# Performance work log

Hardware: AMD Instinct MI355X
Metric: run time of the kernel (lower is better)

Reference implementation:

```python
import jax, jax.numpy as jnp
import numpy as np

N_CIR, N_DIS, D, H = 585, 88, 128, 8
E_CC, E_DD = 20000, 3000
EPS = 1e-16


def _gcn(x, src, dst, ew, W, b, N):
    # PyG GCNConv: add self-loops (weight 1), symmetric normalization, x @ W, scatter-add, + bias
    loop = jnp.arange(N)
    s = jnp.concatenate([src, loop])
    d = jnp.concatenate([dst, loop])
    w = jnp.concatenate([ew, jnp.ones((N,), ew.dtype)])
    deg = jax.ops.segment_sum(w, d, num_segments=N)
    dinv = jnp.where(deg > 0, jax.lax.rsqrt(deg), 0.0)
    norm = dinv[s] * w * dinv[d]                      # [E+N]
    h = x @ W                                         # [N,D]
    out = jax.ops.segment_sum(h[s] * norm[:, None], d, num_segments=N)
    return out + b


def _gat(x, src, dst, ea, W, a_src, a_dst, a_edge, We, b, N):
    # PyG GATConv(heads=H, concat=False, edge_dim=1): self-loops with mean edge_attr fill,
    # leaky_relu attention logits, segment softmax over destination, mean over heads, + bias
    loop = jnp.arange(N)
    s = jnp.concatenate([src, loop])
    d = jnp.concatenate([dst, loop])
    ea = jnp.concatenate([ea, jnp.broadcast_to(ea.mean(0, keepdims=True), (N, ea.shape[1]))], 0)
    h = (x @ W).reshape(N, H, D)                      # [N,H,D]
    e = (ea @ We).reshape(-1, H, D)                   # [E+N,H,D]
    alpha = (h * a_src).sum(-1)[s] + (h * a_dst).sum(-1)[d] + (e * a_edge).sum(-1)
    alpha = jax.nn.leaky_relu(alpha, 0.2)             # [E+N,H]
    amax = jax.ops.segment_max(alpha, d, num_segments=N)
    ex = jnp.exp(alpha - amax[d])
    den = jax.ops.segment_sum(ex, d, num_segments=N)
    alpha = ex / (den[d] + EPS)
    out = jax.ops.segment_sum(h[s] * alpha[:, :, None], d, num_segments=N)  # [N,H,D]
    return out.mean(1) + b


def _branch(x, edges, mat, gw1, gb1, aw, asrc, adst, aedge, awe, ab, gw2, gb2, N):
    src, dst = edges[0], edges[1]
    ew = mat[src, dst]                                # gather edge weights from dense matrix
    f1 = jax.nn.relu(_gcn(x, src, dst, ew, gw1, gb1, N))
    att = jax.nn.relu(_gat(f1, src, dst, ew[:, None], aw, asrc, adst, aedge, awe, ab, N))
    f2 = jax.nn.relu(_gcn(att, src, dst, ew, gw2, gb2, N))
    return f1, f2


def _cnn(f1, f2, Wk, b):
    # Conv2d(2,256,(128,1)) over [1,2,128,N] == per-node GEMM over (2,128) then view/transpose
    Xv = jnp.stack([f1.T, f2.T])                      # [2,D,N]
    return jnp.einsum('ock,ckn->no', Wk[..., 0], Xv) + b  # [N,256]


def setup_inputs():
    ks = jax.random.split(jax.random.key(0), 24)
    rn = lambda i, sh, s=1.0: jax.random.normal(ks[i], sh, jnp.float32) * s
    w = 0.08  # ~glorot scale for fan-in 128
    return {
        'x_cir': rn(0, (N_CIR, D)),
        'x_dis': rn(1, (N_DIS, D)),
        'cc_matrix': jax.random.uniform(ks[2], (N_CIR, N_CIR), jnp.float32),
        'dd_matrix': jax.random.uniform(ks[3], (N_DIS, N_DIS), jnp.float32),
        'gcn_c1_w': rn(4, (D, D), w), 'gcn_c1_b': jnp.zeros((D,), jnp.float32),
        'gat_c_w': rn(5, (D, H * D), w), 'gat_c_asrc': rn(6, (H, D), w),
        'gat_c_adst': rn(7, (H, D), w), 'gat_c_aedge': rn(8, (H, D), w),
        'gat_c_we': rn(9, (1, H * D), w), 'gat_c_b': jnp.zeros((D,), jnp.float32),
        'gcn_c2_w': rn(10, (D, D), w), 'gcn_c2_b': jnp.zeros((D,), jnp.float32),
        'gcn_d1_w': rn(11, (D, D), w), 'gcn_d1_b': jnp.zeros((D,), jnp.float32),
        'gat_d_w': rn(12, (D, H * D), w), 'gat_d_asrc': rn(13, (H, D), w),
        'gat_d_adst': rn(14, (H, D), w), 'gat_d_aedge': rn(15, (H, D), w),
        'gat_d_we': rn(16, (1, H * D), w), 'gat_d_b': jnp.zeros((D,), jnp.float32),
        'gcn_d2_w': rn(17, (D, D), w), 'gcn_d2_b': jnp.zeros((D,), jnp.float32),
        'conv_c_w': rn(18, (256, 2, D, 1), w), 'conv_c_b': jnp.zeros((256,), jnp.float32),
        'conv_d_w': rn(19, (256, 2, D, 1), w), 'conv_d_b': jnp.zeros((256,), jnp.float32),
        'cc_edges': jax.random.randint(ks[20], (2, E_CC), 0, N_CIR),
        'dd_edges': jax.random.randint(ks[21], (2, E_DD), 0, N_DIS),
    }


def reference(x_cir, x_dis, cc_matrix, dd_matrix,
              gcn_c1_w, gcn_c1_b, gat_c_w, gat_c_asrc, gat_c_adst, gat_c_aedge, gat_c_we, gat_c_b,
              gcn_c2_w, gcn_c2_b,
              gcn_d1_w, gcn_d1_b, gat_d_w, gat_d_asrc, gat_d_adst, gat_d_aedge, gat_d_we, gat_d_b,
              gcn_d2_w, gcn_d2_b,
              conv_c_w, conv_c_b, conv_d_w, conv_d_b,
              cc_edges, dd_edges):
    c1, c2 = _branch(x_cir, cc_edges, cc_matrix, gcn_c1_w, gcn_c1_b, gat_c_w, gat_c_asrc,
                     gat_c_adst, gat_c_aedge, gat_c_we, gat_c_b, gcn_c2_w, gcn_c2_b, N_CIR)
    d1, d2 = _branch(x_dis, dd_edges, dd_matrix, gcn_d1_w, gcn_d1_b, gat_d_w, gat_d_asrc,
                     gat_d_adst, gat_d_aedge, gat_d_we, gat_d_b, gcn_d2_w, gcn_d2_b, N_DIS)
    cir_fea = _cnn(c1, c2, conv_c_w, conv_c_b)        # [585,256]
    dis_fea = _cnn(d1, d2, conv_d_w, conv_d_b)        # [88,256]
    return cir_fea @ dis_fea.T, cir_fea, dis_fea
```

## Files before the change

kernel.cpp:

```cpp
#include <hip/hip_runtime.h>

constexpr int NCIR = 585;
constexpr int NDIS = 88;
constexpr int NT   = NCIR + NDIS;
constexpr int DIM  = 128;
constexpr int NH   = 8;
constexpr int ECC  = 20000;
constexpr int EDD  = 3000;
constexpr int ET   = ECC + EDD;
constexpr int CO   = 256;
constexpr int CAP  = 256;
constexpr int F1C  = (NCIR + 3) / 4;
constexpr int F1D  = (NDIS + 3) / 4;
constexpr int NG   = F1C + F1D;
constexpr int GBK  = (ET + 255) / 256;
constexpr int GEMB = (NT + 1) / 2;

__device__ __forceinline__ int decode_cnt(unsigned raw){
  return (int)(raw >= 0xA0000000u ? raw - 0xAAAAAAAAu : raw);
}

struct P {
  const float *x_c, *x_d, *mat_c, *mat_d;
  const float *g1w_c, *g1b_c, *aw_c, *as_c, *ad_c, *ae_c, *we_c, *ab_c, *g2w_c, *g2b_c;
  const float *g1w_d, *g1b_d, *aw_d, *as_d, *ad_d, *ae_d, *we_d, *ab_d, *g2w_d, *g2b_d;
  const float *cw_c, *cb_c, *cw_d, *cb_d;
  const int *csrc, *cdst, *dsrc, *ddst;
  float *hs, *hd, *h, *f1, *hg, *fill_w, *psc, *psd, *wdeg;
  unsigned *cnt;
  int *fill_s;
  float *out_score, *out_cir, *out_dis;
};

__global__ __launch_bounds__(256) void k_gg(P p){
  __shared__ float r0[256], r1[256];
  int b = blockIdx.x, t = threadIdx.x;
  if (b < GBK){
    int e = b * 256 + t;
    float wc = 0.0f, wdv = 0.0f;
    if (e < ET){
      float w; int s, d;
      if (e < ECC){
        s = p.csrc[e]; d = p.cdst[e];
        w = p.mat_c[s * NCIR + d]; wc = w;
      } else {
        int el = e - ECC;
        s = NCIR + p.dsrc[el]; d = NCIR + p.ddst[el];
        w = p.mat_d[(s - NCIR) * NDIS + (d - NCIR)]; wdv = w;
      }
      int pos = decode_cnt(atomicAdd(&p.cnt[d], 1u));
      if (pos < CAP){
        p.fill_s[d * CAP + pos] = s;
        p.fill_w[d * CAP + pos] = w;
      }
      atomicAdd(&p.wdeg[d], w);
    }
    r0[t] = wc; r1[t] = wdv;
    __syncthreads();
    for (int st = 128; st; st >>= 1){
      if (t < st){ r0[t] += r0[t + st]; r1[t] += r1[t + st]; }
      __syncthreads();
    }
    if (t == 0){ p.psc[b] = r0[0]; p.psd[b] = r1[0]; }
  } else {
    int ub = (b - GBK) * 2;
    int n = t >> 7, k = t & 127;
    int u = ub + n;
    bool ok = u < NT;
    if (ok){
      int br = u >= NCIR;
      r0[n * DIM + k] = br ? p.x_d[(u - NCIR) * DIM + k] : p.x_c[u * DIM + k];
    }
    __syncthreads();
    if (ok){
      const float* W = (u >= NCIR) ? p.g1w_d : p.g1w_c;
      float acc = 0.0f;
      #pragma unroll 8
      for (int c = 0; c < DIM; ++c) acc += r0[n * DIM + c] * W[c * DIM + k];
      p.h[u * DIM + k] = acc;
    }
  }
}

__global__ __launch_bounds__(256) void k_aggproj(P p){
  __shared__ int   deg4[4];
  __shared__ float dv4[4];
  __shared__ int   s4[4][CAP];
  __shared__ float nrm4[4][CAP];
  __shared__ float a_sh[4][DIM];
  __shared__ float wred[4][8];
  int b = blockIdx.x, t = threadIdx.x;
  int ng = b >> 2, ct = b & 3;
  int base, count, br;
  if (ng < F1C){ base = ng * 4; count = min(4, NCIR - base); br = 0; }
  else { base = NCIR + (ng - F1C) * 4; count = 4; br = 1; }
  if (t < 4){
    if (t < count){
      int u = base + t;
      deg4[t] = min(decode_cnt(p.cnt[u]), CAP);
      dv4[t]  = rsqrtf(1.0f + p.wdeg[u]);
    } else deg4[t] = 0;
  }
  __syncthreads();
  for (int idx = t; idx < 4 * CAP; idx += 256){
    int nn = idx >> 8, j = idx & (CAP - 1);
    if (j < deg4[nn]){
      int u = base + nn;
      int s = p.fill_s[u * CAP + j];
      s4[nn][j] = s;
      nrm4[nn][j] = rsqrtf(1.0f + p.wdeg[s]) * p.fill_w[u * CAP + j] * dv4[nn];
    }
  }
  __syncthreads();
  const float* B1 = br ? p.g1b_d : p.g1b_c;
  int n2 = t >> 7, k = t & 127;
  for (int r = 0; r < 2; ++r){
    int nn = n2 + r * 2;
    float v = 0.0f;
    if (nn < count){
      int u = base + nn;
      float dvu = dv4[nn];
      float acc = B1[k] + p.h[u * DIM + k] * dvu * dvu;
      int deg = deg4[nn];
      #pragma unroll 4
      for (int j = 0; j < deg; ++j)
        acc += p.h[s4[nn][j] * DIM + k] * nrm4[nn][j];
      if (ct == 0) p.f1[u * DIM + k] = acc;
      v = fmaxf(acc, 0.0f);
    }
    a_sh[nn][k] = v;
  }
  __syncthreads();
  const float* W = (br ? p.aw_d : p.aw_c) + ct * 256 + t;
  float acc[4] = {0.f, 0.f, 0.f, 0.f};
  #pragma unroll 4
  for (int c = 0; c < DIM; ++c){
    float w = W[c * 1024];
    acc[0] += a_sh[0][c] * w; acc[1] += a_sh[1][c] * w;
    acc[2] += a_sh[2][c] * w; acc[3] += a_sh[3][c] * w;
  }
  int col = ct * 256 + t;
  for (int n = 0; n < count; ++n)
    p.hg[(size_t)(base + n) * 1024 + col] = acc[n];
  const float* As = br ? p.as_d : p.as_c;
  const float* Ad = br ? p.ad_d : p.ad_c;
  float av = As[col], dw = Ad[col];
  int w = t >> 6;
  #pragma unroll
  for (int n = 0; n < 4; ++n){
    float sdot = acc[n] * av, ddot = acc[n] * dw;
    #pragma unroll
    for (int off = 32; off; off >>= 1){
      sdot += __shfl_down(sdot, off, 64);
      ddot += __shfl_down(ddot, off, 64);
    }
    if ((t & 63) == 0){ wred[w][n * 2] = sdot; wred[w][n * 2 + 1] = ddot; }
  }
  __syncthreads();
  if (t < 16){
    int g = t >> 3, v = t & 7, n = v >> 1, isd = v & 1;
    if (n < count){
      float sum = wred[g * 2][v] + wred[g * 2 + 1][v];
      float* dst = isd ? p.hd : p.hs;
      dst[(base + n) * NH + ct * 2 + g] = sum;
    }
  }
}

__global__ __launch_bounds__(256) void k_att(P p){
  __shared__ float den_sh[NH], hd_sh[NH], inv_sh[NH], wself_sh[NH], wd_sh[NH];
  __shared__ float slw_sh;
  __shared__ int   s_all[CAP];
  __shared__ float w_all[CAP];
  __shared__ float alpha_all[CAP * NH];
  __shared__ float a2[2][DIM], attv[DIM], part[2][DIM];
  int d = blockIdx.x, t = threadIdx.x;
  int g = t >> 7, k = t & 127;
  int br = d >= NCIR;
  int wv = t >> 6, lane = t & 63;
  if (t < NH){ den_sh[t] = 0.0f; hd_sh[t] = p.hd[d * NH + t]; }
  if (wv == 0){
    const float* ps = br ? p.psd : p.psc;
    float v = (lane < GBK ? ps[lane] : 0.0f) + (lane + 64 < GBK ? ps[lane + 64] : 0.0f);
    #pragma unroll
    for (int off = 32; off; off >>= 1) v += __shfl_down(v, off, 64);
    if (lane == 0) slw_sh = v / (br ? (float)EDD : (float)ECC);
  }
  if (wv >= 2){
    const float* We = br ? p.we_d : p.we_c;
    const float* Ae = br ? p.ae_d : p.ae_c;
    for (int q = 0; q < 4; ++q){
      int hh = (wv - 2) * 4 + q;
      float v = We[hh * DIM + lane] * Ae[hh * DIM + lane]
              + We[hh * DIM + 64 + lane] * Ae[hh * DIM + 64 + lane];
      #pragma unroll
      for (int off = 32; off; off >>= 1) v += __shfl_down(v, off, 64);
      if (lane == 0) wd_sh[hh] = v;
    }
  }
  int deg = min(decode_cnt(p.cnt[d]), CAP);
  for (int j = t; j < deg; j += 256){
    s_all[j] = p.fill_s[d * CAP + j];
    w_all[j] = p.fill_w[d * CAP + j];
  }
  __syncthreads();
  for (int idx = t; idx < deg * NH; idx += 256){
    int j = idx >> 3, hh = idx & 7;
    int s = s_all[j];
    float a = p.hs[s * NH + hh] + hd_sh[hh] + w_all[j] * wd_sh[hh];
    a = a > 0.0f ? a : 0.2f * a;
    float ex = expf(a);
    alpha_all[idx] = ex;
    atomicAdd(&den_sh[hh], ex);
  }
  __syncthreads();
  if (t < NH){
    float a = p.hs[d * NH + t] + hd_sh[t] + slw_sh * wd_sh[t];
    a = a > 0.0f ? a : 0.2f * a;
    float ex = expf(a);
    float inv = 1.0f / (den_sh[t] + ex + 1e-16f) * 0.125f;
    inv_sh[t] = inv;
    wself_sh[t] = ex * inv;
  }
  __syncthreads();
  for (int idx = t; idx < deg * NH; idx += 256)
    alpha_all[idx] *= inv_sh[idx & 7];
  __syncthreads();
  float acc = 0.0f;
  if (g == 0){
    acc = (br ? p.ab_d : p.ab_c)[k];
    const float* r = p.hg + (size_t)d * 1024;
    #pragma unroll
    for (int hh = 0; hh < NH; ++hh) acc += wself_sh[hh] * r[hh * DIM + k];
  }
  for (int jj = g; jj < deg; jj += 2){
    const float* r = p.hg + (size_t)s_all[jj] * 1024;
    const float* al = alpha_all + jj * NH;
    #pragma unroll
    for (int hh = 0; hh < NH; ++hh) acc += al[hh] * r[hh * DIM + k];
  }
  a2[g][k] = acc;
  __syncthreads();
  if (g == 0) attv[k] = fmaxf(a2[0][k] + a2[1][k], 0.0f);
  __syncthreads();
  const float* W = br ? p.g2w_d : p.g2w_c;
  float h2 = 0.0f;
  #pragma unroll 8
  for (int c = g * 64; c < g * 64 + 64; ++c) h2 += attv[c] * W[c * DIM + k];
  part[g][k] = h2;
  __syncthreads();
  if (g == 0) p.h[d * DIM + k] = part[0][k] + part[1][k];
}

__global__ __launch_bounds__(256) void k_fuse2(P p){
  __shared__ float s12[4][2 * DIM];
  __shared__ int   deg4[4];
  __shared__ float dv4[4];
  __shared__ int   s4[4][CAP];
  __shared__ float nrm4[4][CAP];
  int b = blockIdx.x, o = threadIdx.x;
  int gbase, count, br; float* out;
  if (b < F1C){ gbase = b * 4; count = min(4, NCIR - gbase); br = 0;
                out = p.out_cir + (size_t)gbase * CO; }
  else { int lb = (b - F1C) * 4; gbase = NCIR + lb; count = 4; br = 1;
         out = p.out_dis + (size_t)lb * CO; }
  if (o < 4){
    if (o < count){
      int u = gbase + o;
      deg4[o] = min(decode_cnt(p.cnt[u]), CAP);
      dv4[o]  = rsqrtf(1.0f + p.wdeg[u]);
    } else deg4[o] = 0;
  }
  __syncthreads();
  for (int idx = o; idx < 4 * CAP; idx += 256){
    int nn = idx >> 8, j = idx & (CAP - 1);
    if (j < deg4[nn]){
      int u = gbase + nn;
      int s = p.fill_s[u * CAP + j];
      s4[nn][j] = s;
      nrm4[nn][j] = rsqrtf(1.0f + p.wdeg[s]) * p.fill_w[u * CAP + j] * dv4[nn];
    }
  }
  __syncthreads();
  const float* B2 = br ? p.g2b_d : p.g2b_c;
  int n2 = o >> 7, k = o & 127;
  for (int r = 0; r < 2; ++r){
    int nn = n2 + r * 2;
    float v1 = 0.0f, v2 = 0.0f;
    if (nn < count){
      int u = gbase + nn;
      float dvu = dv4[nn];
      float acc = B2[k] + p.h[u * DIM + k] * dvu * dvu;
      int deg = deg4[nn];
      #pragma unroll 4
      for (int j = 0; j < deg; ++j)
        acc += p.h[s4[nn][j] * DIM + k] * nrm4[nn][j];
      v2 = fmaxf(acc, 0.0f);
      v1 = fmaxf(p.f1[u * DIM + k], 0.0f);
    }
    s12[nn][k] = v1;
    s12[nn][DIM + k] = v2;
  }
  __syncthreads();
  const float* W = (br ? p.cw_d : p.cw_c) + o * 2 * DIM;
  float bv = (br ? p.cb_d : p.cb_c)[o];
  float a0 = bv, a1 = bv, a2 = bv, a3 = bv;
  #pragma unroll 4
  for (int q = 0; q < 2 * DIM; ++q){
    float wv = W[q];
    a0 += s12[0][q] * wv; a1 += s12[1][q] * wv;
    a2 += s12[2][q] * wv; a3 += s12[3][q] * wv;
  }
  if (0 < count) out[0 * CO + o] = a0;
  if (1 < count) out[1 * CO + o] = a1;
  if (2 < count) out[2 * CO + o] = a2;
  if (3 < count) out[3 * CO + o] = a3;
}

__global__ void k_final(P p){
  __shared__ float ci[CO];
  int i = blockIdx.x, j = threadIdx.x;
  ci[j]       = p.out_cir[i * CO + j];
  ci[DIM + j] = p.out_cir[i * CO + DIM + j];
  __syncthreads();
  if (j < NDIS){
    const float* dr = p.out_dis + j * CO;
    float acc = 0.0f;
    #pragma unroll 8
    for (int q = 0; q < CO; ++q) acc += ci[q] * dr[q];
    p.out_score[i * NDIS + j] = acc;
  }
}

extern "C" void kernel_launch(void* const* d_in, const int* in_sizes, int n_in,
                              void* d_out, int out_size, void* d_ws, size_t ws_size,
                              hipStream_t stream){
  P p;
  typedef const float* F;
  p.x_c   = (F)d_in[0];  p.x_d   = (F)d_in[1];
  p.mat_c = (F)d_in[2];  p.mat_d = (F)d_in[3];
  p.g1w_c = (F)d_in[4];  p.g1b_c = (F)d_in[5];
  p.aw_c  = (F)d_in[6];  p.as_c  = (F)d_in[7];  p.ad_c = (F)d_in[8];
  p.ae_c  = (F)d_in[9];  p.we_c  = (F)d_in[10]; p.ab_c = (F)d_in[11];
  p.g2w_c = (F)d_in[12]; p.g2b_c = (F)d_in[13];
  p.g1w_d = (F)d_in[14]; p.g1b_d = (F)d_in[15];
  p.aw_d  = (F)d_in[16]; p.as_d  = (F)d_in[17]; p.ad_d = (F)d_in[18];
  p.ae_d  = (F)d_in[19]; p.we_d  = (F)d_in[20]; p.ab_d = (F)d_in[21];
  p.g2w_d = (F)d_in[22]; p.g2b_d = (F)d_in[23];
  p.cw_c  = (F)d_in[24]; p.cb_c  = (F)d_in[25];
  p.cw_d  = (F)d_in[26]; p.cb_d  = (F)d_in[27];
  const int* cc_edges = (const int*)d_in[28];
  const int* dd_edges = (const int*)d_in[29];
  p.csrc = cc_edges;  p.cdst = cc_edges + ECC;
  p.dsrc = dd_edges;  p.ddst = dd_edges + EDD;

  float* out = (float*)d_out;
  p.out_score = out;
  p.out_cir   = out + NCIR * NDIS;
  p.out_dis   = p.out_cir + NCIR * CO;

  float* w = (float*)d_ws;
  auto alloc = [&](size_t n){ float* q = w; w += n; return q; };
  p.wdeg   = alloc(676);
  p.cnt    = (unsigned*)alloc(676);
  p.psc    = alloc(92);
  p.psd    = alloc(92);
  p.hs     = alloc((size_t)NT * NH);
  p.hd     = alloc((size_t)NT * NH);
  p.h      = alloc((size_t)NT * DIM);
  p.f1     = alloc((size_t)NT * DIM);
  p.hg     = alloc((size_t)NT * 1024);
  p.fill_w = alloc((size_t)NT * CAP);
  p.fill_s = (int*)alloc((size_t)NT * CAP);

  k_gg     <<<GBK + GEMB, 256, 0, stream>>>(p);
  k_aggproj<<<NG * 4,     256, 0, stream>>>(p);
  k_att    <<<NT,         256, 0, stream>>>(p);
  k_fuse2  <<<F1C + F1D,  256, 0, stream>>>(p);
  k_final  <<<NCIR,       DIM, 0, stream>>>(p);
}
```

Baseline: 192.4 us.

## Vectorize gathers with float4 and split neighbor loops across warp slots

```diff
diff --git a/kernel.cpp b/kernel.cpp
--- a/kernel.cpp
+++ b/kernel.cpp
@@ -26,7 +26,7 @@
   const float *g1w_d, *g1b_d, *aw_d, *as_d, *ad_d, *ae_d, *we_d, *ab_d, *g2w_d, *g2b_d;
   const float *cw_c, *cb_c, *cw_d, *cb_d;
   const int *csrc, *cdst, *dsrc, *ddst;
-  float *hs, *hd, *h, *f1, *hg, *fill_w, *psc, *psd, *wdeg;
+  float *hs, *hd, *h, *f1, *hg, *fill_w, *psc, *psd, *wdeg, *wdall;
   unsigned *cnt;
   int *fill_s;
   float *out_score, *out_cir, *out_dis;
@@ -62,7 +62,7 @@
       __syncthreads();
     }
     if (t == 0){ p.psc[b] = r0[0]; p.psd[b] = r1[0]; }
-  } else {
+  } else if (b < GBK + GEMB){
     int ub = (b - GBK) * 2;
     int n = t >> 7, k = t & 127;
     int u = ub + n;
@@ -79,6 +79,17 @@
       for (int c = 0; c < DIM; ++c) acc += r0[n * DIM + c] * W[c * DIM + k];
       p.h[u * DIM + k] = acc;
     }
+  } else {
+    int brn = b - (GBK + GEMB);
+    const float* We = brn ? p.we_d : p.we_c;
+    const float* Ae = brn ? p.ae_d : p.ae_c;
+    int hh = t >> 5, l = t & 31;
+    float v = 0.0f;
+    #pragma unroll
+    for (int q = l; q < DIM; q += 32) v += We[hh * DIM + q] * Ae[hh * DIM + q];
+    #pragma unroll
+    for (int off = 16; off; off >>= 1) v += __shfl_down(v, off, 32);
+    if (l == 0) p.wdall[brn * NH + hh] = v;
   }
 }
 
@@ -87,6 +98,7 @@
   __shared__ float dv4[4];
   __shared__ int   s4[4][CAP];
   __shared__ float nrm4[4][CAP];
+  __shared__ __align__(16) float apart[8][DIM];
   __shared__ float a_sh[4][DIM];
   __shared__ float wred[4][8];
   int b = blockIdx.x, t = threadIdx.x;
@@ -112,23 +124,40 @@
     }
   }
   __syncthreads();
-  const float* B1 = br ? p.g1b_d : p.g1b_c;
-  int n2 = t >> 7, k = t & 127;
-  for (int r = 0; r < 2; ++r){
-    int nn = n2 + r * 2;
-    float v = 0.0f;
+  {
+    int slot = t >> 5, lane = t & 31;
+    int nn = slot >> 1, jp = slot & 1;
+    float4 acc4 = {0.f, 0.f, 0.f, 0.f};
     if (nn < count){
-      int u = base + nn;
-      float dvu = dv4[nn];
-      float acc = B1[k] + p.h[u * DIM + k] * dvu * dvu;
+      if (jp == 0){
+        int u = base + nn;
+        float sc = dv4[nn] * dv4[nn];
+        const float4* B14 = (const float4*)(br ? p.g1b_d : p.g1b_c);
+        const float4* h4  = (const float4*)(p.h + (size_t)u * DIM);
+        float4 bb = B14[lane], hv = h4[lane];
+        acc4.x = bb.x + hv.x * sc; acc4.y = bb.y + hv.y * sc;
+        acc4.z = bb.z + hv.z * sc; acc4.w = bb.w + hv.w * sc;
+      }
       int deg = deg4[nn];
-      #pragma unroll 4
-      for (int j = 0; j < deg; ++j)
-        acc += p.h[s4[nn][j] * DIM + k] * nrm4[nn][j];
-      if (ct == 0) p.f1[u * DIM + k] = acc;
-      v = fmaxf(acc, 0.0f);
-    }
-    a_sh[nn][k] = v;
+      for (int j = jp; j < deg; j += 2){
+        const float4* hr = (const float4*)(p.h + (size_t)s4[nn][j] * DIM);
+        float w = nrm4[nn][j];
+        float4 hv = hr[lane];
+        acc4.x += hv.x * w; acc4.y += hv.y * w;
+        acc4.z += hv.z * w; acc4.w += hv.w * w;
+      }
+    }
+    ((float4*)apart[slot])[lane] = acc4;
+  }
+  __syncthreads();
+  {
+    int n2 = t >> 7, k = t & 127;
+    for (int r = 0; r < 2; ++r){
+      int nn = n2 + r * 2;
+      float sum = apart[nn * 2][k] + apart[nn * 2 + 1][k];
+      if (nn < count && ct == 0) p.f1[(size_t)(base + nn) * DIM + k] = sum;
+      a_sh[nn][k] = (nn < count) ? fmaxf(sum, 0.0f) : 0.0f;
+    }
   }
   __syncthreads();
   const float* W = (br ? p.aw_d : p.aw_c) + ct * 256 + t;
@@ -173,30 +202,24 @@
   __shared__ int   s_all[CAP];
   __shared__ float w_all[CAP];
   __shared__ float alpha_all[CAP * NH];
-  __shared__ float a2[2][DIM], attv[DIM], part[2][DIM];
+  __shared__ __align__(16) float hacc[NH][DIM];
+  __shared__ float attv[DIM];
+  __shared__ float part[2][DIM];
   int d = blockIdx.x, t = threadIdx.x;
   int g = t >> 7, k = t & 127;
   int br = d >= NCIR;
-  int wv = t >> 6, lane = t & 63;
-  if (t < NH){ den_sh[t] = 0.0f; hd_sh[t] = p.hd[d * NH + t]; }
+  int wv = t >> 6, lane64 = t & 63;
+  if (t < NH){
+    den_sh[t] = 0.0f;
+    hd_sh[t]  = p.hd[d * NH + t];
+    wd_sh[t]  = p.wdall[br * NH + t];
+  }
   if (wv == 0){
     const float* ps = br ? p.psd : p.psc;
-    float v = (lane < GBK ? ps[lane] : 0.0f) + (lane + 64 < GBK ? ps[lane + 64] : 0.0f);
+    float v = (lane64 < GBK ? ps[lane64] : 0.0f) + (lane64 + 64 < GBK ? ps[lane64 + 64] : 0.0f);
     #pragma unroll
     for (int off = 32; off; off >>= 1) v += __shfl_down(v, off, 64);
-    if (lane == 0) slw_sh = v / (br ? (float)EDD : (float)ECC);
-  }
-  if (wv >= 2){
-    const float* We = br ? p.we_d : p.we_c;
-    const float* Ae = br ? p.ae_d : p.ae_c;
-    for (int q = 0; q < 4; ++q){
-      int hh = (wv - 2) * 4 + q;
-      float v = We[hh * DIM + lane] * Ae[hh * DIM + lane]
-              + We[hh * DIM + 64 + lane] * Ae[hh * DIM + 64 + lane];
-      #pragma unroll
-      for (int off = 32; off; off >>= 1) v += __shfl_down(v, off, 64);
-      if (lane == 0) wd_sh[hh] = v;
-    }
+    if (lane64 == 0) slw_sh = v / (br ? (float)EDD : (float)ECC);
   }
   int deg = min(decode_cnt(p.cnt[d]), CAP);
   for (int j = t; j < deg; j += 256){
@@ -226,22 +249,30 @@
   for (int idx = t; idx < deg * NH; idx += 256)
     alpha_all[idx] *= inv_sh[idx & 7];
   __syncthreads();
-  float acc = 0.0f;
-  if (g == 0){
-    acc = (br ? p.ab_d : p.ab_c)[k];
-    const float* r = p.hg + (size_t)d * 1024;
-    #pragma unroll
-    for (int hh = 0; hh < NH; ++hh) acc += wself_sh[hh] * r[hh * DIM + k];
-  }
-  for (int jj = g; jj < deg; jj += 2){
-    const float* r = p.hg + (size_t)s_all[jj] * 1024;
-    const float* al = alpha_all + jj * NH;
-    #pragma unroll
-    for (int hh = 0; hh < NH; ++hh) acc += al[hh] * r[hh * DIM + k];
-  }
-  a2[g][k] = acc;
-  __syncthreads();
-  if (g == 0) attv[k] = fmaxf(a2[0][k] + a2[1][k], 0.0f);
+  {
+    int hh = t >> 5, lane = t & 31;
+    const float4* rd = (const float4*)(p.hg + (size_t)d * 1024 + hh * DIM);
+    float ws = wself_sh[hh];
+    float4 v = rd[lane];
+    float4 acc4 = {ws * v.x, ws * v.y, ws * v.z, ws * v.w};
+    for (int jj = 0; jj < deg; ++jj){
+      const float4* r = (const float4*)(p.hg + (size_t)s_all[jj] * 1024 + hh * DIM);
+      float a = alpha_all[jj * NH + hh];
+      float4 hv = r[lane];
+      acc4.x += a * hv.x; acc4.y += a * hv.y;
+      acc4.z += a * hv.z; acc4.w += a * hv.w;
+    }
+    ((float4*)hacc[hh])[lane] = acc4;
+  }
+  __syncthreads();
+  {
+    float s0 = hacc[g * 4 + 0][k] + hacc[g * 4 + 1][k]
+             + hacc[g * 4 + 2][k] + hacc[g * 4 + 3][k];
+    part[g][k] = s0;
+  }
+  __syncthreads();
+  if (g == 0)
+    attv[k] = fmaxf((br ? p.ab_d : p.ab_c)[k] + part[0][k] + part[1][k], 0.0f);
   __syncthreads();
   const float* W = br ? p.g2w_d : p.g2w_c;
   float h2 = 0.0f;
@@ -253,83 +284,81 @@
 }
 
 __global__ __launch_bounds__(256) void k_fuse2(P p){
-  __shared__ float s12[4][2 * DIM];
-  __shared__ int   deg4[4];
-  __shared__ float dv4[4];
-  __shared__ int   s4[4][CAP];
-  __shared__ float nrm4[4][CAP];
-  int b = blockIdx.x, o = threadIdx.x;
-  int gbase, count, br; float* out;
-  if (b < F1C){ gbase = b * 4; count = min(4, NCIR - gbase); br = 0;
-                out = p.out_cir + (size_t)gbase * CO; }
-  else { int lb = (b - F1C) * 4; gbase = NCIR + lb; count = 4; br = 1;
-         out = p.out_dis + (size_t)lb * CO; }
-  if (o < 4){
-    if (o < count){
-      int u = gbase + o;
-      deg4[o] = min(decode_cnt(p.cnt[u]), CAP);
-      dv4[o]  = rsqrtf(1.0f + p.wdeg[u]);
-    } else deg4[o] = 0;
-  }
-  __syncthreads();
-  for (int idx = o; idx < 4 * CAP; idx += 256){
-    int nn = idx >> 8, j = idx & (CAP - 1);
-    if (j < deg4[nn]){
-      int u = gbase + nn;
-      int s = p.fill_s[u * CAP + j];
-      s4[nn][j] = s;
-      nrm4[nn][j] = rsqrtf(1.0f + p.wdeg[s]) * p.fill_w[u * CAP + j] * dv4[nn];
-    }
-  }
-  __syncthreads();
-  const float* B2 = br ? p.g2b_d : p.g2b_c;
-  int n2 = o >> 7, k = o & 127;
-  for (int r = 0; r < 2; ++r){
-    int nn = n2 + r * 2;
-    float v1 = 0.0f, v2 = 0.0f;
-    if (nn < count){
-      int u = gbase + nn;
-      float dvu = dv4[nn];
-      float acc = B2[k] + p.h[u * DIM + k] * dvu * dvu;
-      int deg = deg4[nn];
-      #pragma unroll 4
-      for (int j = 0; j < deg; ++j)
-        acc += p.h[s4[nn][j] * DIM + k] * nrm4[nn][j];
-      v2 = fmaxf(acc, 0.0f);
-      v1 = fmaxf(p.f1[u * DIM + k], 0.0f);
-    }
-    s12[nn][k] = v1;
-    s12[nn][DIM + k] = v2;
-  }
-  __syncthreads();
-  const float* W = (br ? p.cw_d : p.cw_c) + o * 2 * DIM;
-  float bv = (br ? p.cb_d : p.cb_c)[o];
-  float a0 = bv, a1 = bv, a2 = bv, a3 = bv;
-  #pragma unroll 4
-  for (int q = 0; q < 2 * DIM; ++q){
-    float wv = W[q];
-    a0 += s12[0][q] * wv; a1 += s12[1][q] * wv;
-    a2 += s12[2][q] * wv; a3 += s12[3][q] * wv;
-  }
-  if (0 < count) out[0 * CO + o] = a0;
-  if (1 < count) out[1 * CO + o] = a1;
-  if (2 < count) out[2 * CO + o] = a2;
-  if (3 < count) out[3 * CO + o] = a3;
+  __shared__ int   s_all[CAP];
+  __shared__ float nrm_all[CAP];
+  __shared__ __align__(16) float red[8][DIM];
+  __shared__ __align__(16) float s12[2 * DIM];
+  int u = blockIdx.x, t = threadIdx.x;
+  int br = u >= NCIR;
+  float* out = br ? p.out_dis + (size_t)(u - NCIR) * CO
+                  : p.out_cir + (size_t)u * CO;
+  int deg = min(decode_cnt(p.cnt[u]), CAP);
+  float dvu = rsqrtf(1.0f + p.wdeg[u]);
+  for (int j = t; j < deg; j += 256){
+    int s = p.fill_s[u * CAP + j];
+    s_all[j] = s;
+    nrm_all[j] = rsqrtf(1.0f + p.wdeg[s]) * p.fill_w[u * CAP + j] * dvu;
+  }
+  __syncthreads();
+  {
+    int slot = t >> 5, lane = t & 31;
+    float4 acc4 = {0.f, 0.f, 0.f, 0.f};
+    if (slot == 0){
+      const float4* B24 = (const float4*)(br ? p.g2b_d : p.g2b_c);
+      const float4* h4  = (const float4*)(p.h + (size_t)u * DIM);
+      float sc = dvu * dvu;
+      float4 bb = B24[lane], hv = h4[lane];
+      acc4.x = bb.x + hv.x * sc; acc4.y = bb.y + hv.y * sc;
+      acc4.z = bb.z + hv.z * sc; acc4.w = bb.w + hv.w * sc;
+    }
+    for (int j = slot; j < deg; j += 8){
+      const float4* hr = (const float4*)(p.h + (size_t)s_all[j] * DIM);
+      float w = nrm_all[j];
+      float4 hv = hr[lane];
+      acc4.x += hv.x * w; acc4.y += hv.y * w;
+      acc4.z += hv.z * w; acc4.w += hv.w * w;
+    }
+    ((float4*)red[slot])[lane] = acc4;
+  }
+  __syncthreads();
+  if (t < DIM){
+    float sum = red[0][t] + red[1][t] + red[2][t] + red[3][t]
+              + red[4][t] + red[5][t] + red[6][t] + red[7][t];
+    s12[DIM + t] = fmaxf(sum, 0.0f);
+    s12[t]       = fmaxf(p.f1[(size_t)u * DIM + t], 0.0f);
+  }
+  __syncthreads();
+  const float4* W4 = (const float4*)((br ? p.cw_d : p.cw_c) + (size_t)t * 2 * DIM);
+  const float4* sv = (const float4*)s12;
+  float acc = (br ? p.cb_d : p.cb_c)[t];
+  #pragma unroll 8
+  for (int q = 0; q < 64; ++q){
+    float4 w = W4[q], s = sv[q];
+    acc += w.x * s.x + w.y * s.y + w.z * s.z + w.w * s.w;
+  }
+  out[t] = acc;
 }
 
 __global__ void k_final(P p){
-  __shared__ float ci[CO];
-  int i = blockIdx.x, j = threadIdx.x;
-  ci[j]       = p.out_cir[i * CO + j];
-  ci[DIM + j] = p.out_cir[i * CO + DIM + j];
-  __syncthreads();
+  __shared__ __align__(16) float ci[CO];
+  __shared__ float fin[2][NDIS];
+  int i = blockIdx.x, t = threadIdx.x;
+  ci[t] = p.out_cir[(size_t)i * CO + t];
+  __syncthreads();
+  int half = t >> 7, j = t & 127;
   if (j < NDIS){
-    const float* dr = p.out_dis + j * CO;
+    const float4* dr = (const float4*)(p.out_dis + (size_t)j * CO + half * DIM);
+    const float4* cc = (const float4*)(ci + half * DIM);
     float acc = 0.0f;
     #pragma unroll 8
-    for (int q = 0; q < CO; ++q) acc += ci[q] * dr[q];
-    p.out_score[i * NDIS + j] = acc;
-  }
+    for (int q = 0; q < 32; ++q){
+      float4 a = cc[q], b = dr[q];
+      acc += a.x * b.x + a.y * b.y + a.z * b.z + a.w * b.w;
+    }
+    fin[half][j] = acc;
+  }
+  __syncthreads();
+  if (t < NDIS) p.out_score[(size_t)i * NDIS + t] = fin[0][t] + fin[1][t];
 }
 
 extern "C" void kernel_launch(void* const* d_in, const int* in_sizes, int n_in,
@@ -365,6 +394,7 @@
   p.cnt    = (unsigned*)alloc(676);
   p.psc    = alloc(92);
   p.psd    = alloc(92);
+  p.wdall  = alloc(16);
   p.hs     = alloc((size_t)NT * NH);
   p.hd     = alloc((size_t)NT * NH);
   p.h      = alloc((size_t)NT * DIM);
@@ -373,9 +403,9 @@
   p.fill_w = alloc((size_t)NT * CAP);
   p.fill_s = (int*)alloc((size_t)NT * CAP);
 
-  k_gg     <<<GBK + GEMB, 256, 0, stream>>>(p);
-  k_aggproj<<<NG * 4,     256, 0, stream>>>(p);
-  k_att    <<<NT,         256, 0, stream>>>(p);
-  k_fuse2  <<<F1C + F1D,  256, 0, stream>>>(p);
-  k_final  <<<NCIR,       DIM, 0, stream>>>(p);
-}
+  k_gg     <<<GBK + GEMB + 2, 256, 0, stream>>>(p);
+  k_aggproj<<<NG * 4,         256, 0, stream>>>(p);
+  k_att    <<<NT,             256, 0, stream>>>(p);
+  k_fuse2  <<<NT,             256, 0, stream>>>(p);
+  k_final  <<<NCIR,           256, 0, stream>>>(p);
+}
```

Result: slower. 199.2 us (+3.6%).
